# Performance work log

Measured on AMD Instinct MI355X. Metric: run time of the kernel, lower is better.

## Reference

```python
import math
import jax, jax.numpy as jnp
import numpy as np

FACTOR = 5

def setup_inputs() -> dict:
    key = jax.random.key(0)
    kq, kk, kv, ki = jax.random.split(key, 4)
    b, h, L, d = 4, 8, 4096, 64
    sample_k = min(L, int(FACTOR * math.log(L + 1)))  # 41
    q = jax.random.normal(kq, (b, h, L, d), dtype=jnp.float32)
    k = jax.random.normal(kk, (b, h, L, d), dtype=jnp.float32)
    v = jax.random.normal(kv, (b, h, L, d), dtype=jnp.float32)
    index_sample = jax.random.randint(ki, (L, sample_k), 0, L, dtype=jnp.int64)
    return {"q": q, "k": k, "v": v, "index_sample": index_sample}

def reference(q, k, v, index_sample):
    b, h, l_q, d = q.shape
    l_k = k.shape[2]
    n_top = min(l_q, int(FACTOR * math.log(l_q + 1)))
    # --- ProbSparse query selection ---
    # k_sample[b,h,q,s,d] = k[b,h,index_sample[q,s],d]  (avoids the O(lq*lk*d) expand)
    k_sample = k[:, :, index_sample, :]                      # (b,h,l_q,sample_k,d)
    qk_sample = jnp.einsum('bhqd,bhqsd->bhqs', q, k_sample)  # (b,h,l_q,sample_k)
    m = qk_sample.max(axis=-1) - qk_sample.mean(axis=-1)     # sparsity measure
    _, top_q = jax.lax.top_k(m, n_top)                       # (b,h,n_top)
    # --- sparse attention on selected queries ---
    q_reduce = jnp.take_along_axis(q, top_q[..., None], axis=2)  # (b,h,n_top,d)
    scale = 1.0 / math.sqrt(d)
    scores = jnp.einsum('bhnd,bhkd->bhnk', q_reduce, k) * scale
    attn = jax.nn.softmax(scores, axis=-1)
    context_top = jnp.einsum('bhnk,bhkd->bhnd', attn, v)
    # --- scatter into mean-initialized context (attn_mask is None path) ---
    context = jnp.broadcast_to(v.mean(axis=2, keepdims=True), (b, h, l_q, d))
    bi = jnp.arange(b)[:, None, None]
    hi = jnp.arange(h)[None, :, None]
    context = context.at[bi, hi, top_q].set(context_top)
    return context
```

## Files before the change

### kernel.cpp

```cpp
#include <hip/hip_runtime.h>
#include <hip/hip_bf16.h>


#define NTOP 41
#define NPAD 48
#define CH 64
#define CAND_CAP 64

typedef __attribute__((ext_vector_type(8))) short bf16x8;
typedef __attribute__((ext_vector_type(4))) float f32x4;

__device__ __forceinline__ unsigned short f2bf(float f) {
    unsigned int x = __float_as_uint(f);
    unsigned int r = (x + 0x7FFFu + ((x >> 16) & 1u)) >> 16;
    return (unsigned short)r;
}
__device__ __forceinline__ unsigned int pack2(float lo, float hi) {
    return ((unsigned int)f2bf(hi) << 16) | f2bf(lo);
}
__device__ __forceinline__ float dot8(const float4& qa, const float4& qb,
                                      const float4& ka, const float4& kb) {
    float p = 0.f;
    p = fmaf(qa.x, ka.x, p); p = fmaf(qa.y, ka.y, p);
    p = fmaf(qa.z, ka.z, p); p = fmaf(qa.w, ka.w, p);
    p = fmaf(qb.x, kb.x, p); p = fmaf(qb.y, kb.y, p);
    p = fmaf(qb.z, kb.z, p); p = fmaf(qb.w, kb.w, p);
    return p;
}
__device__ __forceinline__ float red8(float p) {
    p += __shfl_xor(p, 1);
    p += __shfl_xor(p, 2);
    p += __shfl_xor(p, 4);
    return p;
}

__global__ __launch_bounds__(256) void kA_scores(const float* __restrict__ q,
                                                 const float* __restrict__ k,
                                                 const int* __restrict__ idxs,
                                                 float* __restrict__ m_out) {
    __shared__ int sidx[32 * 41];
    int t = threadIdx.x;
    int lane = t & 63, w = t >> 6;
    int g = lane >> 3, sl = lane & 7;
    int lb = ((blockIdx.x & 7) << 9) + (blockIdx.x >> 3);
    long long qflat = (long long)lb * 32 + w * 8 + g;
    int bh = (int)(qflat >> 12);
    int qi0 = (lb * 32) & 4095;
    for (int i = t; i < 32 * 41; i += 256)
        sidx[i] = idxs[(long long)qi0 * 41 + i] & 4095;
    const float4* q4 = (const float4*)q;
    const float4* k4 = (const float4*)k;
    float4 qa = q4[qflat * 16 + sl * 2];
    float4 qb = q4[qflat * 16 + sl * 2 + 1];
    long long kbase = ((long long)bh << 12) * 16;
    __syncthreads();
    const int* irow = sidx + (w * 8 + g) * 41;
    float maxv = -1e30f, sum = 0.f;
#pragma unroll 2
    for (int g4 = 0; g4 < 10; g4++) {
        int ki0 = irow[g4 * 4 + 0], ki1 = irow[g4 * 4 + 1];
        int ki2 = irow[g4 * 4 + 2], ki3 = irow[g4 * 4 + 3];
        float4 ka0 = k4[kbase + (long long)ki0 * 16 + sl * 2];
        float4 kb0 = k4[kbase + (long long)ki0 * 16 + sl * 2 + 1];
        float4 ka1 = k4[kbase + (long long)ki1 * 16 + sl * 2];
        float4 kb1 = k4[kbase + (long long)ki1 * 16 + sl * 2 + 1];
        float4 ka2 = k4[kbase + (long long)ki2 * 16 + sl * 2];
        float4 kb2 = k4[kbase + (long long)ki2 * 16 + sl * 2 + 1];
        float4 ka3 = k4[kbase + (long long)ki3 * 16 + sl * 2];
        float4 kb3 = k4[kbase + (long long)ki3 * 16 + sl * 2 + 1];
        float p0 = red8(dot8(qa, qb, ka0, kb0));
        float p1 = red8(dot8(qa, qb, ka1, kb1));
        float p2 = red8(dot8(qa, qb, ka2, kb2));
        float p3 = red8(dot8(qa, qb, ka3, kb3));
        maxv = fmaxf(maxv, fmaxf(fmaxf(p0, p1), fmaxf(p2, p3)));
        sum += (p0 + p1) + (p2 + p3);
    }
    {
        int ki = irow[40];
        float4 ka = k4[kbase + (long long)ki * 16 + sl * 2];
        float4 kb = k4[kbase + (long long)ki * 16 + sl * 2 + 1];
        float p = red8(dot8(qa, qb, ka, kb));
        maxv = fmaxf(maxv, p);
        sum += p;
    }
    if (sl == 0) m_out[qflat] = maxv - sum * (1.0f / 41.0f);
}

__global__ __launch_bounds__(256) void kB_topk(const float* __restrict__ m_in,
                                               int* __restrict__ topq) {
    __shared__ unsigned int uvals[4096];
    __shared__ unsigned int hist[256];
    __shared__ unsigned int scal[4];
    __shared__ int candIdx[CAND_CAP];
    __shared__ unsigned int candU[CAND_CAP];
    int bh = blockIdx.x, t = threadIdx.x;
    for (int i = t; i < 4096; i += 256) {
        unsigned int b = __float_as_uint(m_in[bh * 4096 + i]);
        uvals[i] = (b & 0x80000000u) ? ~b : (b | 0x80000000u);
    }
    hist[t] = 0;
    __syncthreads();
    for (int i = t; i < 4096; i += 256) atomicAdd(&hist[uvals[i] >> 24], 1u);
    __syncthreads();
    if (t == 0) {
        unsigned int cum = 0, b1 = 0, ca = 0;
        for (int j = 255; j >= 0; j--) {
            if (cum + hist[j] >= 41u) { b1 = (unsigned)j; ca = cum; break; }
            cum += hist[j];
        }
        scal[0] = b1; scal[1] = ca;
    }
    __syncthreads();
    unsigned int b1 = scal[0];
    hist[t] = 0;
    __syncthreads();
    for (int i = t; i < 4096; i += 256)
        if ((uvals[i] >> 24) == b1) atomicAdd(&hist[(uvals[i] >> 16) & 255u], 1u);
    __syncthreads();
    if (t == 0) {
        unsigned int cum = scal[1], b2 = 0;
        for (int j = 255; j >= 0; j--) {
            if (cum + hist[j] >= 41u) { b2 = (unsigned)j; break; }
            cum += hist[j];
        }
        scal[2] = (b1 << 24) | (b2 << 16);
        scal[3] = 0;
    }
    __syncthreads();
    unsigned int T = scal[2];
    for (int i = t; i < 4096; i += 256) {
        unsigned int u = uvals[i];
        if (u >= T) {
            unsigned int pos = atomicAdd(&scal[3], 1u);
            if (pos < CAND_CAP) { candIdx[pos] = i; candU[pos] = u; }
        }
    }
    __syncthreads();
    if (t < 64) {
        int n = (int)min(scal[3], (unsigned)CAND_CAP);
        unsigned int myU = (t < n) ? candU[t] : 0u;
        int myI = (t < n) ? candIdx[t] : 0x7fffffff;
        for (int it = 0; it < NTOP; it++) {
            unsigned int bu = myU;
            int bi = myI;
            for (int off = 32; off; off >>= 1) {
                unsigned int ou = __shfl_xor(bu, off);
                int oi = __shfl_xor(bi, off);
                if (ou > bu || (ou == bu && oi < bi)) { bu = ou; bi = oi; }
            }
            if (t == 0) topq[bh * NTOP + it] = bi;
            if (myI == bi) { myU = 0u; myI = 0x7fffffff; }
        }
    }
}

__global__ __launch_bounds__(256) void kC1(const float* __restrict__ v,
                                           float* __restrict__ vpart) {
    int bh = blockIdx.x, chn = blockIdx.y, t = threadIdx.x;
    int d = t & 63, r = t >> 6;
    long long base = ((long long)bh << 12) + chn * 256;
    float acc = 0.f;
    for (int i = 0; i < 64; i++) acc += v[(base + i * 4 + r) * 64 + d];
    __shared__ float red[256];
    red[t] = acc;
    __syncthreads();
    if (r == 0) vpart[(bh * 16 + chn) * 64 + d] = red[d] + red[64 + d] + red[128 + d] + red[192 + d];
}

__global__ __launch_bounds__(256) void kD(const float* __restrict__ vpart,
                                          float* __restrict__ out) {
    __shared__ __align__(16) float vm[64];
    int t = threadIdx.x;
    int bh = blockIdx.x >> 6;
    if (t < 64) {
        float s = 0.f;
#pragma unroll
        for (int c = 0; c < 16; c++) s += vpart[(bh * 16 + c) * 64 + t];
        vm[t] = s * (1.0f / 4096.0f);
    }
    __syncthreads();
    long long g0 = (long long)blockIdx.x * 1024 + t;
    float4* out4 = (float4*)out;
#pragma unroll
    for (int i = 0; i < 4; i++) {
        long long gg = g0 + i * 256;
        int d4 = (int)(gg & 15);
        out4[gg] = *(const float4*)(&vm[d4 * 4]);
    }
}

__global__ __launch_bounds__(256) void kE_attn(const float* __restrict__ q,
                                               const float* __restrict__ k,
                                               const float* __restrict__ v,
                                               const int* __restrict__ topq,
                                               float* __restrict__ part, int tl) {
    __shared__ unsigned short qs[NPAD * 72];
    __shared__ unsigned short kpb[CH * 72];
    __shared__ unsigned short vt[64 * 72];
    __shared__ float redM[NPAD * 4];
    __shared__ float redS[NPAD * 4];
    __shared__ float m_i[NPAD], l_i[NPAD], fac[NPAD];

    const int t = threadIdx.x;
    const int tile = blockIdx.x, bh = blockIdx.y;
    const int tiles = gridDim.x;
    const int lane = t & 63, w = t >> 6;
    const int c = lane & 15, quad = lane >> 4;
    const long long bhbase = ((long long)bh) << 12;

    const float4* q4f = (const float4*)q;
    const float4* k4f = (const float4*)k;
    const float4* v4f = (const float4*)v;

    for (int i = t; i < NTOP * 16; i += 256) {
        int n = i >> 4, oc = i & 15;
        int row = topq[bh * NTOP + n];
        float4 val = q4f[(bhbase + row) * 16 + oc];
        uint2 pk;
        pk.x = pack2(val.x * 0.125f, val.y * 0.125f);
        pk.y = pack2(val.z * 0.125f, val.w * 0.125f);
        *(uint2*)(&qs[n * 72 + oc * 4]) = pk;
    }
    for (int i = t; i < 7 * 72; i += 256) qs[NTOP * 72 + i] = 0;
    if (t < NPAD) { m_i[t] = -1e30f; l_i[t] = 0.f; fac[t] = 0.f; }

    f32x4 oacc[3];
#pragma unroll
    for (int qt = 0; qt < 3; qt++) oacc[qt] = (f32x4){0.f, 0.f, 0.f, 0.f};

    const int l0 = tile * tl;
    const int nchunk = tl >> 6;
    for (int ch = 0; ch < nchunk; ch++) {
        const int lb = l0 + ch * CH;
        __syncthreads();
#pragma unroll
        for (int i = 0; i < 4; i++) {
            int idx = i * 256 + t;
            int j = idx >> 4, oc = idx & 15;
            float4 val = k4f[(bhbase + lb + j) * 16 + oc];
            uint2 pk;
            pk.x = pack2(val.x, val.y);
            pk.y = pack2(val.z, val.w);
            *(uint2*)(&kpb[j * 72 + oc * 4]) = pk;
        }
        {
            int jp = t & 31, o = t >> 5;
            float4 a0 = v4f[(bhbase + lb + 2 * jp) * 16 + o * 2];
            float4 a1 = v4f[(bhbase + lb + 2 * jp) * 16 + o * 2 + 1];
            float4 b0 = v4f[(bhbase + lb + 2 * jp + 1) * 16 + o * 2];
            float4 b1 = v4f[(bhbase + lb + 2 * jp + 1) * 16 + o * 2 + 1];
            float av[8] = {a0.x, a0.y, a0.z, a0.w, a1.x, a1.y, a1.z, a1.w};
            float bv[8] = {b0.x, b0.y, b0.z, b0.w, b1.x, b1.y, b1.z, b1.w};
#pragma unroll
            for (int e = 0; e < 8; e++)
                *(unsigned int*)(&vt[(o * 8 + e) * 72 + 2 * jp]) = pack2(av[e], bv[e]);
        }
        __syncthreads();
        f32x4 s[3];
        {
            const bf16x8 bk0 = *(const bf16x8*)(&kpb[(w * 16 + c) * 72 + quad * 8]);
            const bf16x8 bk1 = *(const bf16x8*)(&kpb[(w * 16 + c) * 72 + quad * 8 + 32]);
#pragma unroll
            for (int qt = 0; qt < 3; qt++) {
                const bf16x8 a0 = *(const bf16x8*)(&qs[(qt * 16 + c) * 72 + quad * 8]);
                const bf16x8 a1 = *(const bf16x8*)(&qs[(qt * 16 + c) * 72 + quad * 8 + 32]);
                f32x4 s4 = (f32x4){0.f, 0.f, 0.f, 0.f};
                s4 = __builtin_amdgcn_mfma_f32_16x16x32_bf16(a0, bk0, s4, 0, 0, 0);
                s4 = __builtin_amdgcn_mfma_f32_16x16x32_bf16(a1, bk1, s4, 0, 0, 0);
                s[qt] = s4;
            }
        }
#pragma unroll
        for (int qt = 0; qt < 3; qt++) {
#pragma unroll
            for (int r = 0; r < 4; r++) {
                float x = s[qt][r];
                x = fmaxf(x, __shfl_xor(x, 1));
                x = fmaxf(x, __shfl_xor(x, 2));
                x = fmaxf(x, __shfl_xor(x, 4));
                x = fmaxf(x, __shfl_xor(x, 8));
                if (c == 0) redM[(qt * 16 + quad * 4 + r) * 4 + w] = x;
            }
        }
        __syncthreads();
        if (t < NPAD) {
            float rm = fmaxf(fmaxf(redM[t * 4], redM[t * 4 + 1]),
                             fmaxf(redM[t * 4 + 2], redM[t * 4 + 3]));
            float mo = m_i[t];
            float mn = fmaxf(mo, rm);
            fac[t] = __expf(mo - mn);
            m_i[t] = mn;
        }
        __syncthreads();
#pragma unroll
        for (int qt = 0; qt < 3; qt++) {
#pragma unroll
            for (int r = 0; r < 4; r++) {
                int row = qt * 16 + quad * 4 + r;
                float e = __expf(s[qt][r] - m_i[row]);
                float en = __shfl_xor(e, 1);
                if ((c & 1) == 0)
                    *(unsigned int*)(&kpb[row * 72 + w * 16 + c]) = pack2(e, en);
                float sm = e;
                sm += __shfl_xor(sm, 1);
                sm += __shfl_xor(sm, 2);
                sm += __shfl_xor(sm, 4);
                sm += __shfl_xor(sm, 8);
                if (c == 0) redS[row * 4 + w] = sm;
            }
        }
        __syncthreads();
        if (t < NPAD)
            l_i[t] = l_i[t] * fac[t] +
                     (redS[t * 4] + redS[t * 4 + 1]) + (redS[t * 4 + 2] + redS[t * 4 + 3]);
        {
            const bf16x8 bv0 = *(const bf16x8*)(&vt[(w * 16 + c) * 72 + quad * 8]);
            const bf16x8 bv1 = *(const bf16x8*)(&vt[(w * 16 + c) * 72 + quad * 8 + 32]);
#pragma unroll
            for (int qt = 0; qt < 3; qt++) {
                const bf16x8 a0 = *(const bf16x8*)(&kpb[(qt * 16 + c) * 72 + quad * 8]);
                const bf16x8 a1 = *(const bf16x8*)(&kpb[(qt * 16 + c) * 72 + quad * 8 + 32]);
                f32x4 o = oacc[qt];
                o.x *= fac[qt * 16 + quad * 4 + 0];
                o.y *= fac[qt * 16 + quad * 4 + 1];
                o.z *= fac[qt * 16 + quad * 4 + 2];
                o.w *= fac[qt * 16 + quad * 4 + 3];
                o = __builtin_amdgcn_mfma_f32_16x16x32_bf16(a0, bv0, o, 0, 0, 0);
                o = __builtin_amdgcn_mfma_f32_16x16x32_bf16(a1, bv1, o, 0, 0, 0);
                oacc[qt] = o;
            }
        }
    }
    __syncthreads();
    long long pbase = ((long long)(bh * tiles + tile)) * NTOP * 66;
    if (t < NTOP) {
        part[pbase + t * 66 + 0] = m_i[t];
        part[pbase + t * 66 + 1] = l_i[t];
    }
#pragma unroll
    for (int qt = 0; qt < 3; qt++) {
#pragma unroll
        for (int r = 0; r < 4; r++) {
            int n = qt * 16 + quad * 4 + r;
            if (n < NTOP) part[pbase + (long long)n * 66 + 2 + w * 16 + c] = oacc[qt][r];
        }
    }
}

__global__ __launch_bounds__(256) void kF_combine(const float* __restrict__ part,
                                                  const int* __restrict__ topq,
                                                  float* __restrict__ out, int tiles) {
    int t = threadIdx.x;
    int bh = blockIdx.x;
    int n = blockIdx.y * 4 + (t >> 6);
    int d = t & 63;
    if (n >= NTOP) return;
    long long base = ((long long)(bh * tiles)) * NTOP * 66 + (long long)n * 66;
    const long long ts = (long long)NTOP * 66;
    float M = -1e30f;
    for (int tt = 0; tt < tiles; tt++) M = fmaxf(M, part[base + tt * ts]);
    float L = 0.f, acc = 0.f;
    for (int tt = 0; tt < tiles; tt++) {
        float mt = part[base + tt * ts];
        float wgt = __expf(mt - M);
        L += part[base + tt * ts + 1] * wgt;
        acc += part[base + tt * ts + 2 + d] * wgt;
    }
    int row = topq[bh * NTOP + n];
    out[(((long long)bh << 12) + row) * 64 + d] = acc / L;
}

extern "C" void kernel_launch(void* const* d_in, const int* in_sizes, int n_in,
                              void* d_out, int out_size, void* d_ws, size_t ws_size,
                              hipStream_t stream) {
    const float* q = (const float*)d_in[0];
    const float* k = (const float*)d_in[1];
    const float* v = (const float*)d_in[2];
    const int* idxs = (const int*)d_in[3];
    float* out = (float*)d_out;

    char* ws = (char*)d_ws;
    int* ws_topq = (int*)ws;
    float* ws_vpart = (float*)(ws + 8192);
    float* ws_m = (float*)(ws + 147456);
    float* ws_part = (float*)(ws + 147456);

    size_t need16 = 147456ull + 16ull * 32 * NTOP * 66 * 4;
    int tiles = (ws_size >= need16) ? 16 : 8;
    int tl = 4096 / tiles;

    kA_scores<<<4096, 256, 0, stream>>>(q, k, idxs, ws_m);
    kB_topk<<<32, 256, 0, stream>>>(ws_m, ws_topq);
    kC1<<<dim3(32, 16), 256, 0, stream>>>(v, ws_vpart);
    kD<<<2048, 256, 0, stream>>>(ws_vpart, out);
    kE_attn<<<dim3(tiles, 32), 256, 0, stream>>>(q, k, v, ws_topq, ws_part, tl);
    kF_combine<<<dim3(32, 11), 256, 0, stream>>>(ws_part, ws_topq, out, tiles);
}
```

Baseline: 266.4 us.

## Merge six kernel launches into three with last-block combine and skip-overwritten broadcast

Result: slower. 369.5 us (+38.7%).

```diff
diff --git a/kernel.cpp b/kernel.cpp
--- a/kernel.cpp
+++ b/kernel.cpp
@@ -34,15 +34,35 @@
     return p;
 }
 
-__global__ __launch_bounds__(256) void kA_scores(const float* __restrict__ q,
-                                                 const float* __restrict__ k,
-                                                 const int* __restrict__ idxs,
-                                                 float* __restrict__ m_out) {
-    __shared__ int sidx[32 * 41];
-    int t = threadIdx.x;
+__global__ __launch_bounds__(256) void P1_scores_vsum(const float* __restrict__ q,
+                                                      const float* __restrict__ k,
+                                                      const float* __restrict__ v,
+                                                      const int* __restrict__ idxs,
+                                                      float* __restrict__ m_out,
+                                                      float* __restrict__ vpart) {
+    __shared__ __align__(16) char smem[5632];
+    const int t = threadIdx.x;
+    const int bid = blockIdx.x;
+
+    if (bid >= 4096) {
+        float* red = (float*)smem;
+        int cb = bid - 4096;
+        int bh = cb >> 4, chn = cb & 15;
+        int d = t & 63, r = t >> 6;
+        long long base = ((long long)bh << 12) + chn * 256;
+        float acc = 0.f;
+        for (int i = 0; i < 64; i++) acc += v[(base + i * 4 + r) * 64 + d];
+        red[t] = acc;
+        __syncthreads();
+        if (r == 0)
+            vpart[(bh * 16 + chn) * 64 + d] = red[d] + red[64 + d] + red[128 + d] + red[192 + d];
+        return;
+    }
+
+    int* sidx = (int*)smem;
     int lane = t & 63, w = t >> 6;
     int g = lane >> 3, sl = lane & 7;
-    int lb = ((blockIdx.x & 7) << 9) + (blockIdx.x >> 3);
+    int lb = ((bid & 7) << 9) + (bid >> 3);
     long long qflat = (long long)lb * 32 + w * 8 + g;
     int bh = (int)(qflat >> 12);
     int qi0 = (lb * 32) & 4095;
@@ -87,13 +107,15 @@
 }
 
 __global__ __launch_bounds__(256) void kB_topk(const float* __restrict__ m_in,
-                                               int* __restrict__ topq) {
+                                               int* __restrict__ topq,
+                                               unsigned int* __restrict__ cnt) {
     __shared__ unsigned int uvals[4096];
     __shared__ unsigned int hist[256];
     __shared__ unsigned int scal[4];
     __shared__ int candIdx[CAND_CAP];
     __shared__ unsigned int candU[CAND_CAP];
     int bh = blockIdx.x, t = threadIdx.x;
+    if (t == 0) cnt[bh] = 0u;
     for (int i = t; i < 4096; i += 256) {
         unsigned int b = __float_as_uint(m_in[bh * 4096 + i]);
         uvals[i] = (b & 0x80000000u) ? ~b : (b | 0x80000000u);
@@ -154,56 +176,60 @@
     }
 }
 
-__global__ __launch_bounds__(256) void kC1(const float* __restrict__ v,
-                                           float* __restrict__ vpart) {
-    int bh = blockIdx.x, chn = blockIdx.y, t = threadIdx.x;
-    int d = t & 63, r = t >> 6;
-    long long base = ((long long)bh << 12) + chn * 256;
-    float acc = 0.f;
-    for (int i = 0; i < 64; i++) acc += v[(base + i * 4 + r) * 64 + d];
-    __shared__ float red[256];
-    red[t] = acc;
-    __syncthreads();
-    if (r == 0) vpart[(bh * 16 + chn) * 64 + d] = red[d] + red[64 + d] + red[128 + d] + red[192 + d];
-}
-
-__global__ __launch_bounds__(256) void kD(const float* __restrict__ vpart,
-                                          float* __restrict__ out) {
-    __shared__ __align__(16) float vm[64];
-    int t = threadIdx.x;
-    int bh = blockIdx.x >> 6;
-    if (t < 64) {
-        float s = 0.f;
-#pragma unroll
-        for (int c = 0; c < 16; c++) s += vpart[(bh * 16 + c) * 64 + t];
-        vm[t] = s * (1.0f / 4096.0f);
-    }
-    __syncthreads();
-    long long g0 = (long long)blockIdx.x * 1024 + t;
-    float4* out4 = (float4*)out;
-#pragma unroll
-    for (int i = 0; i < 4; i++) {
-        long long gg = g0 + i * 256;
-        int d4 = (int)(gg & 15);
-        out4[gg] = *(const float4*)(&vm[d4 * 4]);
-    }
-}
-
-__global__ __launch_bounds__(256) void kE_attn(const float* __restrict__ q,
-                                               const float* __restrict__ k,
-                                               const float* __restrict__ v,
-                                               const int* __restrict__ topq,
-                                               float* __restrict__ part, int tl) {
+__global__ __launch_bounds__(256) void P3_attn_bcast(const float* __restrict__ q,
+                                                     const float* __restrict__ k,
+                                                     const float* __restrict__ v,
+                                                     const int* __restrict__ topq,
+                                                     const float* __restrict__ vpart,
+                                                     float* __restrict__ part,
+                                                     float* __restrict__ out,
+                                                     unsigned int* __restrict__ cnt,
+                                                     int tiles, int tl) {
     __shared__ unsigned short qs[NPAD * 72];
     __shared__ unsigned short kpb[CH * 72];
     __shared__ unsigned short vt[64 * 72];
     __shared__ float redM[NPAD * 4];
     __shared__ float redS[NPAD * 4];
     __shared__ float m_i[NPAD], l_i[NPAD], fac[NPAD];
+    __shared__ __align__(16) float vm[64];
+    __shared__ unsigned char flag[64];
+    __shared__ int lastFlag;
 
     const int t = threadIdx.x;
-    const int tile = blockIdx.x, bh = blockIdx.y;
-    const int tiles = gridDim.x;
+    const int bid = blockIdx.x;
+    const int nE = tiles * 32;
+
+    if (bid >= nE) {
+        int gb = bid - nE;
+        int bh = gb >> 6;
+        if (t < 64) {
+            float s = 0.f;
+#pragma unroll
+            for (int c = 0; c < 16; c++) s += vpart[(bh * 16 + c) * 64 + t];
+            vm[t] = s * (1.0f / 4096.0f);
+            flag[t] = 0;
+        }
+        __syncthreads();
+        if (t < NTOP) {
+            int r = topq[bh * NTOP + t] - ((gb & 63) << 6);
+            if (r >= 0 && r < 64) flag[r] = 1;
+        }
+        __syncthreads();
+        long long g0 = (long long)gb * 1024 + t;
+        float4* out4 = (float4*)out;
+#pragma unroll
+        for (int i = 0; i < 4; i++) {
+            long long gg = g0 + i * 256;
+            if (!flag[(int)((gg >> 4) & 63)]) {
+                int d4 = (int)(gg & 15);
+                out4[gg] = *(const float4*)(&vm[d4 * 4]);
+            }
+        }
+        return;
+    }
+
+    const int xcd = bid & 7, sub = (bid >> 3) & 3, tile = bid >> 5;
+    const int bh = (xcd << 2) | sub;
     const int lane = t & 63, w = t >> 6;
     const int c = lane & 15, quad = lane >> 4;
     const long long bhbase = ((long long)bh) << 12;
@@ -345,29 +371,35 @@
             if (n < NTOP) part[pbase + (long long)n * 66 + 2 + w * 16 + c] = oacc[qt][r];
         }
     }
-}
-
-__global__ __launch_bounds__(256) void kF_combine(const float* __restrict__ part,
-                                                  const int* __restrict__ topq,
-                                                  float* __restrict__ out, int tiles) {
-    int t = threadIdx.x;
-    int bh = blockIdx.x;
-    int n = blockIdx.y * 4 + (t >> 6);
-    int d = t & 63;
-    if (n >= NTOP) return;
-    long long base = ((long long)(bh * tiles)) * NTOP * 66 + (long long)n * 66;
+
+    __syncthreads();
+    if (t == 0) {
+        __threadfence();
+        unsigned int o = atomicAdd(&cnt[bh], 1u);
+        lastFlag = (o == (unsigned)(tiles - 1));
+    }
+    __syncthreads();
+    if (!lastFlag) return;
+    __threadfence();
+
+    const int d = t & 63;
     const long long ts = (long long)NTOP * 66;
-    float M = -1e30f;
-    for (int tt = 0; tt < tiles; tt++) M = fmaxf(M, part[base + tt * ts]);
-    float L = 0.f, acc = 0.f;
-    for (int tt = 0; tt < tiles; tt++) {
-        float mt = part[base + tt * ts];
-        float wgt = __expf(mt - M);
-        L += part[base + tt * ts + 1] * wgt;
-        acc += part[base + tt * ts + 2 + d] * wgt;
-    }
-    int row = topq[bh * NTOP + n];
-    out[(((long long)bh << 12) + row) * 64 + d] = acc / L;
+    for (int bn = 0; bn < 44; bn += 4) {
+        int n = bn + (t >> 6);
+        if (n >= NTOP) break;
+        long long base = ((long long)(bh * tiles)) * ts + (long long)n * 66;
+        float M = -1e30f;
+        for (int tt = 0; tt < tiles; tt++) M = fmaxf(M, part[base + tt * ts]);
+        float L = 0.f, acc = 0.f;
+        for (int tt = 0; tt < tiles; tt++) {
+            float mt = part[base + tt * ts];
+            float wgt = __expf(mt - M);
+            L += part[base + tt * ts + 1] * wgt;
+            acc += part[base + tt * ts + 2 + d] * wgt;
+        }
+        int row = topq[bh * NTOP + n];
+        out[(((long long)bh << 12) + row) * 64 + d] = acc / L;
+    }
 }
 
 extern "C" void kernel_launch(void* const* d_in, const int* in_sizes, int n_in,
@@ -382,6 +414,7 @@
     char* ws = (char*)d_ws;
     int* ws_topq = (int*)ws;
     float* ws_vpart = (float*)(ws + 8192);
+    unsigned int* ws_cnt = (unsigned int*)(ws + 139264);
     float* ws_m = (float*)(ws + 147456);
     float* ws_part = (float*)(ws + 147456);
 
@@ -389,10 +422,8 @@
     int tiles = (ws_size >= need16) ? 16 : 8;
     int tl = 4096 / tiles;
 
-    kA_scores<<<4096, 256, 0, stream>>>(q, k, idxs, ws_m);
-    kB_topk<<<32, 256, 0, stream>>>(ws_m, ws_topq);
-    kC1<<<dim3(32, 16), 256, 0, stream>>>(v, ws_vpart);
-    kD<<<2048, 256, 0, stream>>>(ws_vpart, out);
-    kE_attn<<<dim3(tiles, 32), 256, 0, stream>>>(q, k, v, ws_topq, ws_part, tl);
-    kF_combine<<<dim3(32, 11), 256, 0, stream>>>(ws_part, ws_topq, out, tiles);
-}
+    P1_scores_vsum<<<4096 + 512, 256, 0, stream>>>(q, k, v, idxs, ws_m, ws_vpart);
+    kB_topk<<<32, 256, 0, stream>>>(ws_m, ws_topq, ws_cnt);
+    P3_attn_bcast<<<tiles * 32 + 2048, 256, 0, stream>>>(q, k, v, ws_topq, ws_vpart,
+                                                         ws_part, out, ws_cnt, tiles, tl);
+}
```
